# Optimization experiments

Measured on AMD Instinct MI355X. Metric: run time of the kernel, lower is better.

## Reference

```python
import jax, jax.numpy as jnp
import numpy as np

N_NODES = 50000


def _gcn_norm(edge_index, num_nodes):
    # add self loops, compute symmetric normalization D^-1/2 (A+I) D^-1/2
    loops = jnp.arange(num_nodes, dtype=edge_index.dtype)
    row = jnp.concatenate([edge_index[0], loops])
    col = jnp.concatenate([edge_index[1], loops])
    deg = jax.ops.segment_sum(jnp.ones_like(row, dtype=jnp.float32), col,
                              num_segments=num_nodes)
    dinv = jnp.where(deg > 0, jax.lax.rsqrt(deg), 0.0)
    norm = dinv[row] * dinv[col]  # [E']
    return row, col, norm


def _gcn_conv(x, W, b, row, col, norm, num_nodes):
    h = x @ W                       # [N, out] transform first (smaller dim)
    msg = h[row] * norm[:, None]    # gather along source nodes  [E', out]
    agg = jax.ops.segment_sum(msg, col, num_segments=num_nodes)  # scatter-add
    return agg + b


def setup_inputs() -> dict:
    key = jax.random.key(0)
    k1, k2, k3, k4 = jax.random.split(key, 4)
    x = jax.random.normal(k1, (N_NODES, 128), dtype=jnp.float32)
    edge_index = jax.random.randint(k2, (2, 800000), 0, N_NODES, dtype=jnp.int64)
    W1 = jax.random.normal(k3, (128, 128), dtype=jnp.float32) * (1.0 / np.sqrt(128))
    b1 = jnp.zeros((128,), dtype=jnp.float32)
    W2 = jax.random.normal(k4, (128, 16), dtype=jnp.float32) * (1.0 / np.sqrt(128))
    b2 = jnp.zeros((16,), dtype=jnp.float32)
    return {"x": x, "edge_index": edge_index, "W1": W1, "b1": b1, "W2": W2, "b2": b2}


def reference(x, edge_index, W1, b1, W2, b2):
    n = x.shape[0]
    row, col, norm = _gcn_norm(edge_index, n)
    h = _gcn_conv(x, W1, b1, row, col, norm, n)
    h = jax.nn.relu(h)
    h = _gcn_conv(h, W2, b2, row, col, norm, n)
    return jax.nn.log_softmax(h, axis=1)
```

## Files before the change

kernel.cpp:

```cpp
#include <hip/hip_runtime.h>
#include <math.h>

constexpr int N  = 50000;
constexpr int E  = 800000;
constexpr int F1 = 128;
constexpr int F2 = 16;
constexpr int BSHIFT  = 8;
constexpr int NBUCKET = (N + 255) >> BSHIFT;
constexpr int CHUNK   = 2048;
constexpr int CAP     = 6144;
constexpr int SBLK    = (E + CHUNK - 1) / CHUNK;
constexpr int GBLK    = 391;

typedef unsigned short ushort_t;
typedef unsigned char  uchar_t;
typedef __bf16 bf16x8 __attribute__((ext_vector_type(8)));
typedef float  f32x4  __attribute__((ext_vector_type(4)));

static __device__ __forceinline__ float blo(unsigned u) { return __uint_as_float(u << 16); }
static __device__ __forceinline__ float bhi(unsigned u) { return __uint_as_float(u & 0xffff0000u); }
static __device__ __forceinline__ ushort_t to_bf(float f) { __bf16 h = (__bf16)f; return *(ushort_t*)&h; }
static __device__ __forceinline__ uchar_t to_fp8(float f) {
    return (uchar_t)(__builtin_amdgcn_cvt_pk_fp8_f32(f, f, 0, false) & 0xff);
}

__global__ __launch_bounds__(256) void k_scatterP_gemm1(const int* __restrict__ row,
                                                        const int* __restrict__ col,
                                                        int* __restrict__ cursor,
                                                        unsigned* __restrict__ P,
                                                        const float* __restrict__ x,
                                                        const float* __restrict__ W1,
                                                        uchar_t* __restrict__ h1q) {
    __shared__ ushort_t Wl[F1 * 136];
    int t = threadIdx.x;

    if (blockIdx.x < SBLK) {
        int* hist = (int*)Wl;
        int* cur  = hist + NBUCKET;
        if (t < NBUCKET) hist[t] = 0;
        __syncthreads();
        int base = blockIdx.x * CHUNK;
#pragma unroll
        for (int i = 0; i < CHUNK / 256; ++i) {
            int e = base + i * 256 + t;
            if (e < E) atomicAdd(&hist[col[e] >> BSHIFT], 1);
        }
        __syncthreads();
        if (t < NBUCKET) cur[t] = t * CAP + atomicAdd(&cursor[t], hist[t]);
        __syncthreads();
#pragma unroll
        for (int i = 0; i < CHUNK / 256; ++i) {
            int e = base + i * 256 + t;
            if (e < E) {
                int c = col[e];
                int pos = atomicAdd(&cur[c >> BSHIFT], 1);
                P[pos] = ((unsigned)row[e] << BSHIFT) | (unsigned)(c & 255);
            }
        }
        return;
    }

    int gb = blockIdx.x - SBLK;
    {
        int n = t & 127, kh = t >> 7;
#pragma unroll
        for (int j = 0; j < 8; ++j) {
            int k0 = (kh * 8 + j) * 8;
            bf16x8 w;
#pragma unroll
            for (int i2 = 0; i2 < 8; ++i2) w[i2] = (__bf16)W1[(k0 + i2) * F1 + n];
            *(bf16x8*)&Wl[n * 136 + k0] = w;
        }
    }
    __syncthreads();

    int lane = t & 63, wv = t >> 6;
    int quad = lane >> 4, l15 = lane & 15;
#pragma unroll 1
    for (int tile = gb * 2; tile < gb * 2 + 2; ++tile) {
        int arow = tile * 64 + wv * 16 + l15;
        int rclamp = min(arow, N - 1);
        f32x4 acc[8] = {};
#pragma unroll
        for (int kk = 0; kk < 4; ++kk) {
            int k0 = kk * 32 + quad * 8;
            const float* xp = x + (size_t)rclamp * F1 + k0;
            float4 u0 = *(const float4*)xp;
            float4 u1 = *(const float4*)(xp + 4);
            bf16x8 a;
            a[0] = (__bf16)u0.x; a[1] = (__bf16)u0.y; a[2] = (__bf16)u0.z; a[3] = (__bf16)u0.w;
            a[4] = (__bf16)u1.x; a[5] = (__bf16)u1.y; a[6] = (__bf16)u1.z; a[7] = (__bf16)u1.w;
#pragma unroll
            for (int ct = 0; ct < 8; ++ct) {
                bf16x8 b = *(const bf16x8*)&Wl[(ct * 16 + l15) * 136 + k0];
                acc[ct] = __builtin_amdgcn_mfma_f32_16x16x32_bf16(a, b, acc[ct], 0, 0, 0);
            }
        }
        int orow0 = tile * 64 + wv * 16 + quad * 4;
#pragma unroll
        for (int r = 0; r < 4; ++r) {
            int orow = orow0 + r;
            if (orow < N) {
#pragma unroll
                for (int ct = 0; ct < 8; ++ct)
                    h1q[(size_t)orow * F1 + ct * 16 + l15] = to_fp8(acc[ct][r]);
            }
        }
    }
}

__global__ __launch_bounds__(512) void k_binFinal(const unsigned* __restrict__ P,
                                                  const int* __restrict__ cursor,
                                                  ushort_t* __restrict__ csr16,
                                                  int* __restrict__ seg_start,
                                                  int* __restrict__ counts,
                                                  float* __restrict__ dinv) {
    __shared__ unsigned eb[CAP];
    __shared__ int cnt[256];
    __shared__ int cur[256];
    __shared__ int wtot[4];
    int t = threadIdx.x;
    int b = blockIdx.x;
    int lo = b << BSHIFT;
    int n_nodes = min(256, N - lo);
    int m = cursor[b];
    if (t < 256) cnt[t] = 0;
    __syncthreads();
    const unsigned* Pb = P + (size_t)b * CAP;
    for (int k = t; k < m; k += 512) {
        unsigned u = Pb[k];
        eb[k] = u;
        atomicAdd(&cnt[u & 255], 1);
    }
    __syncthreads();
    int lane = t & 63, wid = t >> 6;
    int v = 0, incl = 0;
    if (t < 256) {
        v = cnt[t];
        incl = v;
#pragma unroll
        for (int d = 1; d < 64; d <<= 1) {
            int u = __shfl_up(incl, d, 64);
            if (lane >= d) incl += u;
        }
        if (lane == 63) wtot[wid] = incl;
    }
    __syncthreads();
    if (t < 256) {
        int wb = 0;
        for (int w = 0; w < wid; ++w) wb += wtot[w];
        int o = b * CAP + wb + incl - v;
        cur[t] = o;
        if (t < n_nodes) {
            seg_start[lo + t] = o;
            counts[lo + t] = v;
            dinv[lo + t] = rsqrtf((float)v + 1.f);
        }
    }
    __syncthreads();
    for (int k = t; k < m; k += 512) {
        unsigned u = eb[k];
        int pos = atomicAdd(&cur[u & 255], 1);
        csr16[pos] = (ushort_t)(u >> BSHIFT);
    }
}

__global__ __launch_bounds__(256) void k_gather1_gemm2(const uchar_t* __restrict__ h1q,
                                                       const int* __restrict__ seg_start,
                                                       const int* __restrict__ counts,
                                                       const ushort_t* __restrict__ csr16,
                                                       const float* __restrict__ dinv,
                                                       const float* __restrict__ W2,
                                                       const float* __restrict__ b1,
                                                       ushort_t* __restrict__ h2s) {
    __shared__ ushort_t W2l[F2 * 136];
    __shared__ ushort_t T[16 * 136];
    __shared__ float dv[16];
    int t = threadIdx.x;
    for (int i = t; i < F1 * F2; i += 256) {
        int k = i >> 4, n = i & 15;
        W2l[n * 136 + k] = to_bf(W2[i]);
    }
    int lane = t & 63, wv = t >> 6;
    int half = lane >> 5, q = lane & 31;
    float4 bb = ((const float4*)b1)[q];
    int nbase = blockIdx.x * 16;

#define G1LOAD(n_, u_) { int jj = j + half + 2 * (u_); int src = min(jj, rem - 1);          \
        int r = __shfl(rl, src); float ee = __shfl(dl, src); if (jj >= rem) ee = 0.f;       \
        w##n_ = *(const unsigned*)(h1q + (size_t)r * F1 + (q << 2)); e##n_ = ee; }
#define G1ACC(n_) { a0 = fmaf(e##n_, __builtin_amdgcn_cvt_f32_fp8(w##n_, 0), a0);           \
                    a1 = fmaf(e##n_, __builtin_amdgcn_cvt_f32_fp8(w##n_, 1), a1);           \
                    a2 = fmaf(e##n_, __builtin_amdgcn_cvt_f32_fp8(w##n_, 2), a2);           \
                    a3 = fmaf(e##n_, __builtin_amdgcn_cvt_f32_fp8(w##n_, 3), a3); }

#pragma unroll 1
    for (int i = 0; i < 4; ++i) {
        int nl = wv * 4 + i;
        int c = nbase + nl;
        float a0 = 0.f, a1 = 0.f, a2 = 0.f, a3 = 0.f;
        float dc = 0.f;
        if (c < N) {
            dc = dinv[c];
            int s = seg_start[c];
            int cntc = counts[c];
            for (int s0 = 0; s0 < cntc; s0 += 64) {
                int rem = min(cntc - s0, 64);
                int rl = 0; float dl = 0.f;
                if (lane < rem) { rl = csr16[s + s0 + lane]; dl = dinv[rl]; }
#pragma unroll 1
                for (int j = 0; j < rem; j += 16) {
                    unsigned w0, w1, w2, w3, w4, w5, w6, w7;
                    float e0, e1, e2, e3, e4, e5, e6, e7;
                    G1LOAD(0, 0) G1LOAD(1, 1) G1LOAD(2, 2) G1LOAD(3, 3)
                    G1LOAD(4, 4) G1LOAD(5, 5) G1LOAD(6, 6) G1LOAD(7, 7)
                    G1ACC(0) G1ACC(1) G1ACC(2) G1ACC(3)
                    G1ACC(4) G1ACC(5) G1ACC(6) G1ACC(7)
                }
            }
            a0 += __shfl_xor(a0, 32); a1 += __shfl_xor(a1, 32);
            a2 += __shfl_xor(a2, 32); a3 += __shfl_xor(a3, 32);
            unsigned us = *(const unsigned*)(h1q + (size_t)c * F1 + (q << 2));
            a0 = fmaf(dc, __builtin_amdgcn_cvt_f32_fp8(us, 0), a0);
            a1 = fmaf(dc, __builtin_amdgcn_cvt_f32_fp8(us, 1), a1);
            a2 = fmaf(dc, __builtin_amdgcn_cvt_f32_fp8(us, 2), a2);
            a3 = fmaf(dc, __builtin_amdgcn_cvt_f32_fp8(us, 3), a3);
            a0 = fmaxf(fmaf(dc, a0, bb.x), 0.f);
            a1 = fmaxf(fmaf(dc, a1, bb.y), 0.f);
            a2 = fmaxf(fmaf(dc, a2, bb.z), 0.f);
            a3 = fmaxf(fmaf(dc, a3, bb.w), 0.f);
        }
        if (half == 0) {
            unsigned p0 = (unsigned)to_bf(a0) | ((unsigned)to_bf(a1) << 16);
            unsigned p1 = (unsigned)to_bf(a2) | ((unsigned)to_bf(a3) << 16);
            uint2 pp; pp.x = p0; pp.y = p1;
            *(uint2*)&T[nl * 136 + (q << 2)] = pp;
        }
        if (lane == 0) dv[nl] = dc;
    }
#undef G1LOAD
#undef G1ACC
    __syncthreads();

    if (wv == 0) {
        int quad = lane >> 4, l15 = lane & 15;
        f32x4 acc = {};
#pragma unroll
        for (int kk = 0; kk < 4; ++kk) {
            int k0 = kk * 32 + quad * 8;
            bf16x8 a = *(const bf16x8*)&T[l15 * 136 + k0];
            bf16x8 b = *(const bf16x8*)&W2l[l15 * 136 + k0];
            acc = __builtin_amdgcn_mfma_f32_16x16x32_bf16(a, b, acc, 0, 0, 0);
        }
#pragma unroll
        for (int r = 0; r < 4; ++r) {
            int rw = quad * 4 + r;
            int gn = nbase + rw;
            if (gn < N) h2s[(size_t)gn * F2 + l15] = to_bf(acc[r] * dv[rw]);
        }
    }
}

__global__ __launch_bounds__(256) void k_gather2(const ushort_t* __restrict__ h2s,
                                                 const int* __restrict__ seg_start,
                                                 const int* __restrict__ counts,
                                                 const ushort_t* __restrict__ csr16,
                                                 const float* __restrict__ dinv,
                                                 const float* __restrict__ b2,
                                                 float* __restrict__ out) {
    int idx = blockIdx.x * 256 + threadIdx.x;
    int node = idx >> 3, sub = idx & 7;
    if (node >= N) return;
    int lane = threadIdx.x & 63;
    int gb = lane & 56;
    int s = seg_start[node], cntc = counts[node];
    float ax = 0.f, ay = 0.f;

#define G2LOAD(n_) { int src = gb | min(n_, rem - 1); int r = __shfl(rl, src);              \
        w##n_ = ((const unsigned*)(h2s + (size_t)r * F2))[sub]; if (n_ >= rem) w##n_ = 0u; }

#pragma unroll 1
    for (int j0 = 0; j0 < cntc; j0 += 8) {
        int rem = min(cntc - j0, 8);
        int rl = 0;
        if (sub < rem) rl = csr16[s + j0 + sub];
        unsigned w0, w1, w2, w3, w4, w5, w6, w7;
        G2LOAD(0) G2LOAD(1) G2LOAD(2) G2LOAD(3)
        G2LOAD(4) G2LOAD(5) G2LOAD(6) G2LOAD(7)
        ax += ((blo(w0) + blo(w1)) + (blo(w2) + blo(w3))) +
              ((blo(w4) + blo(w5)) + (blo(w6) + blo(w7)));
        ay += ((bhi(w0) + bhi(w1)) + (bhi(w2) + bhi(w3))) +
              ((bhi(w4) + bhi(w5)) + (bhi(w6) + bhi(w7)));
    }
#undef G2LOAD
    unsigned us = ((const unsigned*)(h2s + (size_t)node * F2))[sub];
    ax += blo(us);
    ay += bhi(us);
    float dc = dinv[node];
    float2 bb = ((const float2*)b2)[sub];
    float v0 = fmaf(dc, ax, bb.x);
    float v1 = fmaf(dc, ay, bb.y);
    float mx = fmaxf(v0, v1);
#pragma unroll
    for (int m = 1; m < 8; m <<= 1) mx = fmaxf(mx, __shfl_xor(mx, m));
    float sm = expf(v0 - mx) + expf(v1 - mx);
#pragma unroll
    for (int m = 1; m < 8; m <<= 1) sm += __shfl_xor(sm, m);
    float lse = mx + logf(sm);
    float2 o;
    o.x = v0 - lse;
    o.y = v1 - lse;
    ((float2*)(out + (size_t)node * F2))[sub] = o;
}

extern "C" void kernel_launch(void* const* d_in, const int* in_sizes, int n_in,
                              void* d_out, int out_size, void* d_ws, size_t ws_size,
                              hipStream_t stream) {
    const float* x  = (const float*)d_in[0];
    const int*   ei = (const int*)d_in[1];
    const float* W1 = (const float*)d_in[2];
    const float* b1 = (const float*)d_in[3];
    const float* W2 = (const float*)d_in[4];
    const float* b2 = (const float*)d_in[5];
    const int* row = ei;
    const int* col = ei + E;

    char* ws = (char*)d_ws;
    int*      cursor    = (int*)ws;      ws += 256 * 4;
    unsigned* P         = (unsigned*)ws; ws += (size_t)NBUCKET * CAP * 4;
    ushort_t* csr16     = (ushort_t*)ws; ws += (size_t)NBUCKET * CAP * 2;
    int*      seg_start = (int*)ws;      ws += (size_t)N * 4;
    int*      counts    = (int*)ws;      ws += (size_t)N * 4;
    float*    dinv      = (float*)ws;    ws += (size_t)N * 4;
    uchar_t*  h1q       = (uchar_t*)ws;  ws += (size_t)N * F1;
    ushort_t* h2s       = (ushort_t*)ws; ws += (size_t)N * F2 * 2;

    hipMemsetAsync(cursor, 0, 256 * 4, stream);

    k_scatterP_gemm1<<<SBLK + GBLK, 256, 0, stream>>>(row, col, cursor, P, x, W1, h1q);
    k_binFinal<<<NBUCKET, 512, 0, stream>>>(P, cursor, csr16, seg_start, counts, dinv);
    k_gather1_gemm2<<<(N + 15) / 16, 256, 0, stream>>>(h1q, seg_start, counts, csr16,
                                                       dinv, W2, b1, h2s);
    k_gather2<<<((size_t)N * 8 + 255) / 256, 256, 0, stream>>>(h2s, seg_start, counts, csr16,
                                                               dinv, b2, (float*)d_out);
}
```

Before: 154.9 us.

## Process four nodes per wave in layer-1 gather and pad global bucket cursors

The layer-1 gather now assigns 16 lanes to each destination node, so a wave handles four nodes at once instead of looping over them serially. Each lane reads 8 fp8 features per neighbor, and the neighbor index and its bf16 dinv are packed into one word for the shuffle. The global bucket cursors are spaced 32 ints apart to reduce atomic contention on shared cache lines, and col values are cached in registers so they are not reloaded in the scatter pass. The cost is lane imbalance, since every node group in a wave loops to the largest degree, and the neighbor dinv is rounded to bf16.

```diff
diff --git a/kernel.cpp b/kernel.cpp
--- a/kernel.cpp
+++ b/kernel.cpp
@@ -11,6 +11,7 @@
 constexpr int CAP     = 6144;
 constexpr int SBLK    = (E + CHUNK - 1) / CHUNK;
 constexpr int GBLK    = 391;
+constexpr int CSTRIDE = 32;
 
 typedef unsigned short ushort_t;
 typedef unsigned char  uchar_t;
@@ -22,6 +23,10 @@
 static __device__ __forceinline__ ushort_t to_bf(float f) { __bf16 h = (__bf16)f; return *(ushort_t*)&h; }
 static __device__ __forceinline__ uchar_t to_fp8(float f) {
     return (uchar_t)(__builtin_amdgcn_cvt_pk_fp8_f32(f, f, 0, false) & 0xff);
+}
+template <int S>
+static __device__ __forceinline__ float cf8(unsigned u) {
+    return __builtin_amdgcn_cvt_f32_fp8(u, S);
 }
 
 __global__ __launch_bounds__(256) void k_scatterP_gemm1(const int* __restrict__ row,
@@ -40,19 +45,21 @@
         if (t < NBUCKET) hist[t] = 0;
         __syncthreads();
         int base = blockIdx.x * CHUNK;
+        int ce[CHUNK / 256];
 #pragma unroll
         for (int i = 0; i < CHUNK / 256; ++i) {
             int e = base + i * 256 + t;
-            if (e < E) atomicAdd(&hist[col[e] >> BSHIFT], 1);
+            ce[i] = (e < E) ? col[e] : -1;
+            if (ce[i] >= 0) atomicAdd(&hist[ce[i] >> BSHIFT], 1);
         }
         __syncthreads();
-        if (t < NBUCKET) cur[t] = t * CAP + atomicAdd(&cursor[t], hist[t]);
+        if (t < NBUCKET) cur[t] = t * CAP + atomicAdd(&cursor[t * CSTRIDE], hist[t]);
         __syncthreads();
 #pragma unroll
         for (int i = 0; i < CHUNK / 256; ++i) {
             int e = base + i * 256 + t;
-            if (e < E) {
-                int c = col[e];
+            if (ce[i] >= 0) {
+                int c = ce[i];
                 int pos = atomicAdd(&cur[c >> BSHIFT], 1);
                 P[pos] = ((unsigned)row[e] << BSHIFT) | (unsigned)(c & 255);
             }
@@ -123,7 +130,7 @@
     int b = blockIdx.x;
     int lo = b << BSHIFT;
     int n_nodes = min(256, N - lo);
-    int m = cursor[b];
+    int m = cursor[b * CSTRIDE];
     if (t < 256) cnt[t] = 0;
     __syncthreads();
     const unsigned* Pb = P + (size_t)b * CAP;
@@ -173,8 +180,8 @@
                                                        const float* __restrict__ W2,
                                                        const float* __restrict__ b1,
                                                        ushort_t* __restrict__ h2s) {
-    __shared__ ushort_t W2l[F2 * 136];
-    __shared__ ushort_t T[16 * 136];
+    __shared__ __align__(16) ushort_t W2l[F2 * 136];
+    __shared__ __align__(16) ushort_t T[16 * 136];
     __shared__ float dv[16];
     int t = threadIdx.x;
     for (int i = t; i < F1 * F2; i += 256) {
@@ -182,68 +189,84 @@
         W2l[n * 136 + k] = to_bf(W2[i]);
     }
     int lane = t & 63, wv = t >> 6;
-    int half = lane >> 5, q = lane & 31;
-    float4 bb = ((const float4*)b1)[q];
-    int nbase = blockIdx.x * 16;
-
-#define G1LOAD(n_, u_) { int jj = j + half + 2 * (u_); int src = min(jj, rem - 1);          \
-        int r = __shfl(rl, src); float ee = __shfl(dl, src); if (jj >= rem) ee = 0.f;       \
-        w##n_ = *(const unsigned*)(h1q + (size_t)r * F1 + (q << 2)); e##n_ = ee; }
-#define G1ACC(n_) { a0 = fmaf(e##n_, __builtin_amdgcn_cvt_f32_fp8(w##n_, 0), a0);           \
-                    a1 = fmaf(e##n_, __builtin_amdgcn_cvt_f32_fp8(w##n_, 1), a1);           \
-                    a2 = fmaf(e##n_, __builtin_amdgcn_cvt_f32_fp8(w##n_, 2), a2);           \
-                    a3 = fmaf(e##n_, __builtin_amdgcn_cvt_f32_fp8(w##n_, 3), a3); }
+    int g = lane >> 4, l15 = lane & 15;
+    int gbase = lane & 48;
+    int nl = wv * 4 + g;
+    int c = blockIdx.x * 16 + nl;
+    int cl = min(c, N - 1);
+
+    float dc = 0.f;
+    int s = seg_start[cl];
+    int cnt = 0;
+    if (c < N) { dc = dinv[c]; cnt = counts[c]; }
+    int mcnt = cnt;
+    mcnt = max(mcnt, __shfl_xor(mcnt, 16));
+    mcnt = max(mcnt, __shfl_xor(mcnt, 32));
+
+    float a0 = 0.f, a1 = 0.f, a2 = 0.f, a3 = 0.f;
+    float a4 = 0.f, a5 = 0.f, a6 = 0.f, a7 = 0.f;
+
+#define G1FLT(j_, jb_) { unsigned u = __shfl(pk, gbase + (jb_) + (j_));                     \
+        e##j_ = __uint_as_float(u & 0xffff0000u);                                           \
+        w##j_ = *(const uint2*)(h1q + ((size_t)(u & 0xffffu) << 7) + (l15 << 3)); }
+#define G1ACC(j_) {                                                                         \
+        a0 = fmaf(e##j_, cf8<0>(w##j_.x), a0); a1 = fmaf(e##j_, cf8<1>(w##j_.x), a1);       \
+        a2 = fmaf(e##j_, cf8<2>(w##j_.x), a2); a3 = fmaf(e##j_, cf8<3>(w##j_.x), a3);       \
+        a4 = fmaf(e##j_, cf8<0>(w##j_.y), a4); a5 = fmaf(e##j_, cf8<1>(w##j_.y), a5);       \
+        a6 = fmaf(e##j_, cf8<2>(w##j_.y), a6); a7 = fmaf(e##j_, cf8<3>(w##j_.y), a7); }
 
 #pragma unroll 1
-    for (int i = 0; i < 4; ++i) {
-        int nl = wv * 4 + i;
-        int c = nbase + nl;
-        float a0 = 0.f, a1 = 0.f, a2 = 0.f, a3 = 0.f;
-        float dc = 0.f;
-        if (c < N) {
-            dc = dinv[c];
-            int s = seg_start[c];
-            int cntc = counts[c];
-            for (int s0 = 0; s0 < cntc; s0 += 64) {
-                int rem = min(cntc - s0, 64);
-                int rl = 0; float dl = 0.f;
-                if (lane < rem) { rl = csr16[s + s0 + lane]; dl = dinv[rl]; }
-#pragma unroll 1
-                for (int j = 0; j < rem; j += 16) {
-                    unsigned w0, w1, w2, w3, w4, w5, w6, w7;
-                    float e0, e1, e2, e3, e4, e5, e6, e7;
-                    G1LOAD(0, 0) G1LOAD(1, 1) G1LOAD(2, 2) G1LOAD(3, 3)
-                    G1LOAD(4, 4) G1LOAD(5, 5) G1LOAD(6, 6) G1LOAD(7, 7)
-                    G1ACC(0) G1ACC(1) G1ACC(2) G1ACC(3)
-                    G1ACC(4) G1ACC(5) G1ACC(6) G1ACC(7)
-                }
-            }
-            a0 += __shfl_xor(a0, 32); a1 += __shfl_xor(a1, 32);
-            a2 += __shfl_xor(a2, 32); a3 += __shfl_xor(a3, 32);
-            unsigned us = *(const unsigned*)(h1q + (size_t)c * F1 + (q << 2));
-            a0 = fmaf(dc, __builtin_amdgcn_cvt_f32_fp8(us, 0), a0);
-            a1 = fmaf(dc, __builtin_amdgcn_cvt_f32_fp8(us, 1), a1);
-            a2 = fmaf(dc, __builtin_amdgcn_cvt_f32_fp8(us, 2), a2);
-            a3 = fmaf(dc, __builtin_amdgcn_cvt_f32_fp8(us, 3), a3);
-            a0 = fmaxf(fmaf(dc, a0, bb.x), 0.f);
-            a1 = fmaxf(fmaf(dc, a1, bb.y), 0.f);
-            a2 = fmaxf(fmaf(dc, a2, bb.z), 0.f);
-            a3 = fmaxf(fmaf(dc, a3, bb.w), 0.f);
-        }
-        if (half == 0) {
-            unsigned p0 = (unsigned)to_bf(a0) | ((unsigned)to_bf(a1) << 16);
-            unsigned p1 = (unsigned)to_bf(a2) | ((unsigned)to_bf(a3) << 16);
-            uint2 pp; pp.x = p0; pp.y = p1;
-            *(uint2*)&T[nl * 136 + (q << 2)] = pp;
-        }
-        if (lane == 0) dv[nl] = dc;
-    }
-#undef G1LOAD
+    for (int k0 = 0; k0 < mcnt; k0 += 16) {
+        unsigned pk = 0;
+        int k = k0 + l15;
+        if (k < cnt) {
+            int r = csr16[s + k];
+            pk = ((unsigned)to_bf(dinv[r]) << 16) | (unsigned)r;
+        }
+        {
+            uint2 w0, w1, w2, w3, w4, w5, w6, w7;
+            float e0, e1, e2, e3, e4, e5, e6, e7;
+            G1FLT(0, 0) G1FLT(1, 0) G1FLT(2, 0) G1FLT(3, 0)
+            G1FLT(4, 0) G1FLT(5, 0) G1FLT(6, 0) G1FLT(7, 0)
+            G1ACC(0) G1ACC(1) G1ACC(2) G1ACC(3)
+            G1ACC(4) G1ACC(5) G1ACC(6) G1ACC(7)
+        }
+        if (k0 + 8 < mcnt) {
+            uint2 w0, w1, w2, w3, w4, w5, w6, w7;
+            float e0, e1, e2, e3, e4, e5, e6, e7;
+            G1FLT(0, 8) G1FLT(1, 8) G1FLT(2, 8) G1FLT(3, 8)
+            G1FLT(4, 8) G1FLT(5, 8) G1FLT(6, 8) G1FLT(7, 8)
+            G1ACC(0) G1ACC(1) G1ACC(2) G1ACC(3)
+            G1ACC(4) G1ACC(5) G1ACC(6) G1ACC(7)
+        }
+    }
+#undef G1FLT
 #undef G1ACC
+
+    {
+        uint2 ws = *(const uint2*)(h1q + ((size_t)cl << 7) + (l15 << 3));
+        a0 = fmaf(dc, cf8<0>(ws.x), a0); a1 = fmaf(dc, cf8<1>(ws.x), a1);
+        a2 = fmaf(dc, cf8<2>(ws.x), a2); a3 = fmaf(dc, cf8<3>(ws.x), a3);
+        a4 = fmaf(dc, cf8<0>(ws.y), a4); a5 = fmaf(dc, cf8<1>(ws.y), a5);
+        a6 = fmaf(dc, cf8<2>(ws.y), a6); a7 = fmaf(dc, cf8<3>(ws.y), a7);
+        float4 bL = ((const float4*)b1)[l15 * 2];
+        float4 bH = ((const float4*)b1)[l15 * 2 + 1];
+        a0 = fmaxf(fmaf(dc, a0, bL.x), 0.f); a1 = fmaxf(fmaf(dc, a1, bL.y), 0.f);
+        a2 = fmaxf(fmaf(dc, a2, bL.z), 0.f); a3 = fmaxf(fmaf(dc, a3, bL.w), 0.f);
+        a4 = fmaxf(fmaf(dc, a4, bH.x), 0.f); a5 = fmaxf(fmaf(dc, a5, bH.y), 0.f);
+        a6 = fmaxf(fmaf(dc, a6, bH.z), 0.f); a7 = fmaxf(fmaf(dc, a7, bH.w), 0.f);
+        uint4 pp;
+        pp.x = (unsigned)to_bf(a0) | ((unsigned)to_bf(a1) << 16);
+        pp.y = (unsigned)to_bf(a2) | ((unsigned)to_bf(a3) << 16);
+        pp.z = (unsigned)to_bf(a4) | ((unsigned)to_bf(a5) << 16);
+        pp.w = (unsigned)to_bf(a6) | ((unsigned)to_bf(a7) << 16);
+        *(uint4*)&T[nl * 136 + (l15 << 3)] = pp;
+        if (l15 == 0) dv[nl] = dc;
+    }
     __syncthreads();
 
     if (wv == 0) {
-        int quad = lane >> 4, l15 = lane & 15;
+        int quad = lane >> 4;
         f32x4 acc = {};
 #pragma unroll
         for (int kk = 0; kk < 4; ++kk) {
@@ -255,7 +278,7 @@
 #pragma unroll
         for (int r = 0; r < 4; ++r) {
             int rw = quad * 4 + r;
-            int gn = nbase + rw;
+            int gn = blockIdx.x * 16 + rw;
             if (gn < N) h2s[(size_t)gn * F2 + l15] = to_bf(acc[r] * dv[rw]);
         }
     }
@@ -326,7 +349,7 @@
     const int* col = ei + E;
 
     char* ws = (char*)d_ws;
-    int*      cursor    = (int*)ws;      ws += 256 * 4;
+    int*      cursor    = (int*)ws;      ws += 256 * CSTRIDE * 4;
     unsigned* P         = (unsigned*)ws; ws += (size_t)NBUCKET * CAP * 4;
     ushort_t* csr16     = (ushort_t*)ws; ws += (size_t)NBUCKET * CAP * 2;
     int*      seg_start = (int*)ws;      ws += (size_t)N * 4;
@@ -335,7 +358,7 @@
     uchar_t*  h1q       = (uchar_t*)ws;  ws += (size_t)N * F1;
     ushort_t* h2s       = (ushort_t*)ws; ws += (size_t)N * F2 * 2;
 
-    hipMemsetAsync(cursor, 0, 256 * 4, stream);
+    (void)hipMemsetAsync(cursor, 0, 256 * CSTRIDE * 4, stream);
 
     k_scatterP_gemm1<<<SBLK + GBLK, 256, 0, stream>>>(row, col, cursor, P, x, W1, h1q);
     k_binFinal<<<NBUCKET, 512, 0, stream>>>(P, cursor, csr16, seg_start, counts, dinv);
```

Result: faster. 142.9 us (-7.8%).
